# Performance work log

Hardware: AMD Instinct MI355X
Metric: run time of the kernel (lower is better)

## Reference

```python
import jax, jax.numpy as jnp
import numpy as np

N = 10000
E = 80000


def gat_layer(x, src, dst, W, a_src, a_dst, b):
    # x: [N, Fin], W: [Fin, Fout]
    xw = x @ W                              # [N, Fout]
    al_src = xw @ a_src                     # [N]
    al_dst = xw @ a_dst                     # [N]
    e = jax.nn.leaky_relu(al_src[src] + al_dst[dst], 0.2)  # [E+N]
    m = jax.lax.stop_gradient(jax.ops.segment_max(e, dst, num_segments=N))
    ex = jnp.exp(e - m[dst])
    denom = jax.ops.segment_sum(ex, dst, num_segments=N)
    alpha = ex / (denom[dst] + 1e-16)       # PyG softmax eps
    out = jax.ops.segment_sum(alpha[:, None] * xw[src], dst, num_segments=N)
    return out + b


def setup_inputs() -> dict:
    key = jax.random.key(0)
    ks = jax.random.split(key, 12)
    x = jax.random.normal(ks[0], (N, 256), dtype=jnp.float32)
    edge_index = jax.random.randint(ks[1], (2, E), 0, N, dtype=jnp.int64)
    def glorot(k, fi, fo):
        return jax.random.normal(k, (fi, fo), jnp.float32) * jnp.sqrt(2.0 / (fi + fo))
    W1 = glorot(ks[2], 256, 2048)
    W2 = glorot(ks[3], 2048, 2048)
    W3 = glorot(ks[4], 2048, 1024)
    a1s = jax.random.normal(ks[5], (2048,), jnp.float32) * 0.05
    a1d = jax.random.normal(ks[6], (2048,), jnp.float32) * 0.05
    a2s = jax.random.normal(ks[7], (2048,), jnp.float32) * 0.05
    a2d = jax.random.normal(ks[8], (2048,), jnp.float32) * 0.05
    a3s = jax.random.normal(ks[9], (1024,), jnp.float32) * 0.05
    a3d = jax.random.normal(ks[10], (1024,), jnp.float32) * 0.05
    b1 = jnp.zeros((2048,), jnp.float32)
    b2 = jnp.zeros((2048,), jnp.float32)
    b3 = jnp.zeros((1024,), jnp.float32)
    return {"x": x, "edge_index": edge_index, "W1": W1, "W2": W2, "W3": W3,
            "a1s": a1s, "a1d": a1d, "a2s": a2s, "a2d": a2d, "a3s": a3s, "a3d": a3d,
            "b1": b1, "b2": b2, "b3": b3}


def reference(x, edge_index, W1, W2, W3, a1s, a1d, a2s, a2d, a3s, a3d, b1, b2, b3):
    # add self loops (PyG GATConv default add_self_loops=True)
    loop = jnp.arange(N, dtype=edge_index.dtype)
    src = jnp.concatenate([edge_index[0], loop])
    dst = jnp.concatenate([edge_index[1], loop])
    h = jax.nn.relu(gat_layer(x, src, dst, W1, a1s, a1d, b1))
    h = jax.nn.relu(gat_layer(h, src, dst, W2, a2s, a2d, b2))
    h = jax.nn.relu(gat_layer(h, src, dst, W3, a3s, a3d, b3))
    # F.normalize(dim=1), eps=1e-12
    norm = jnp.linalg.norm(h, axis=1, keepdims=True)
    return h / jnp.maximum(norm, 1e-12)
```

## Files before the change

kernel.cpp:

```cpp
#include <hip/hip_runtime.h>
#include <hip/hip_bf16.h>
#include <math.h>


typedef __attribute__((ext_vector_type(8))) short short8;
typedef __attribute__((ext_vector_type(4))) float f32x4;

#define GLOAD_LDS16(g, l)                                            \
  __builtin_amdgcn_global_load_lds(                                  \
      (const __attribute__((address_space(1))) void*)(g),            \
      (__attribute__((address_space(3))) void*)(l), 16, 0, 0)

#define CFENCE asm volatile("" ::: "memory")

__device__ __forceinline__ float bf16_to_f32(ushort u) {
  return __uint_as_float(((unsigned int)u) << 16);
}

__device__ __forceinline__ float block_reduce_sum_bcast(float v) {
#pragma unroll
  for (int off = 32; off > 0; off >>= 1) v += __shfl_down(v, off, 64);
  __shared__ float tmp[4];
  __shared__ float res;
  int lane = threadIdx.x & 63, w = threadIdx.x >> 6;
  if (lane == 0) tmp[w] = v;
  __syncthreads();
  if (threadIdx.x == 0) res = tmp[0] + tmp[1] + tmp[2] + tmp[3];
  __syncthreads();
  float out = res;
  __syncthreads();
  return out;
}

__device__ __forceinline__ float block_reduce_max_bcast(float v) {
#pragma unroll
  for (int off = 32; off > 0; off >>= 1) v = fmaxf(v, __shfl_down(v, off, 64));
  __shared__ float tmpm[4];
  __shared__ float resm;
  int lane = threadIdx.x & 63, w = threadIdx.x >> 6;
  if (lane == 0) tmpm[w] = v;
  __syncthreads();
  if (threadIdx.x == 0) resm = fmaxf(fmaxf(tmpm[0], tmpm[1]), fmaxf(tmpm[2], tmpm[3]));
  __syncthreads();
  float out = resm;
  __syncthreads();
  return out;
}

__global__ void detect_kernel(const int* __restrict__ ei32, int* __restrict__ flag) {
  __shared__ int cnt;
  if (threadIdx.x == 0) cnt = 0;
  __syncthreads();
  int zeros = 0;
  for (int i = threadIdx.x; i < 1024; i += 256) {
    if (ei32[2 * i + 1] == 0) zeros++;
  }
  atomicAdd(&cnt, zeros);
  __syncthreads();
  if (threadIdx.x == 0) *flag = (cnt > 900) ? 1 : 0;
}

__global__ void convert_kernel(const void* __restrict__ ei, const int* __restrict__ flag,
                               int E, int* __restrict__ src, int* __restrict__ dst) {
  int i = blockIdx.x * blockDim.x + threadIdx.x;
  if (i >= E) return;
  if (*flag) {
    const long long* p = (const long long*)ei;
    src[i] = (int)p[i];
    dst[i] = (int)p[E + i];
  } else {
    const int* p = (const int*)ei;
    src[i] = p[i];
    dst[i] = p[E + i];
  }
}

__global__ __launch_bounds__(256) void convert_f32_bf16(const float* __restrict__ in,
                                                        __hip_bfloat16* __restrict__ out,
                                                        int n) {
  int i = blockIdx.x * blockDim.x + threadIdx.x;
  if (i < n) out[i] = __float2bfloat16(in[i]);
}

__global__ __launch_bounds__(256) void transpose_w(const float* __restrict__ W,
                                                   __hip_bfloat16* __restrict__ Wt,
                                                   int K, int Nout) {
  __shared__ float t[32][33];
  int tx = threadIdx.x & 31, ty = threadIdx.x >> 5;
  int n0 = blockIdx.x * 32, k0 = blockIdx.y * 32;
#pragma unroll
  for (int i = 0; i < 4; ++i) {
    int k = k0 + ty + i * 8;
    t[ty + i * 8][tx] = W[(size_t)k * Nout + n0 + tx];
  }
  __syncthreads();
#pragma unroll
  for (int i = 0; i < 4; ++i) {
    int n = n0 + ty + i * 8;
    Wt[(size_t)n * K + k0 + tx] = __float2bfloat16(t[tx][ty + i * 8]);
  }
}

__global__ __launch_bounds__(256) void matvec_wa(const float* __restrict__ W,
                                                 const float* __restrict__ a_s,
                                                 const float* __restrict__ a_d,
                                                 float* __restrict__ wa_s,
                                                 float* __restrict__ wa_d, int F) {
  int k = blockIdx.x;
  const float* row = W + (size_t)k * F;
  float s1 = 0.f, s2 = 0.f;
  for (int f = threadIdx.x; f < F; f += 256) {
    float w = row[f];
    s1 += w * a_s[f];
    s2 += w * a_d[f];
  }
  float r1 = block_reduce_sum_bcast(s1);
  float r2 = block_reduce_sum_bcast(s2);
  if (threadIdx.x == 0) {
    wa_s[k] = r1;
    wa_d[k] = r2;
  }
}

template <int FPT>
__global__ __launch_bounds__(256) void compute_al(const ushort* __restrict__ H,
                                                  const float* __restrict__ wa_s,
                                                  const float* __restrict__ wa_d,
                                                  float* __restrict__ als,
                                                  float* __restrict__ ald, int F) {
  int n = blockIdx.x;
  const ushort* row = H + (size_t)n * F;
  float s1 = 0.f, s2 = 0.f;
  if (FPT == 8) {
    int base = threadIdx.x * 8;
    short8 v = *(const short8*)(row + base);
#pragma unroll
    for (int j = 0; j < 8; ++j) {
      float f = bf16_to_f32((ushort)v[j]);
      s1 += f * wa_s[base + j];
      s2 += f * wa_d[base + j];
    }
  } else {
    float f = bf16_to_f32(row[threadIdx.x]);
    s1 = f * wa_s[threadIdx.x];
    s2 = f * wa_d[threadIdx.x];
  }
  float r1 = block_reduce_sum_bcast(s1);
  float r2 = block_reduce_sum_bcast(s2);
  if (threadIdx.x == 0) {
    als[n] = r1;
    ald[n] = r2;
  }
}

__global__ void count_kernel(const int* __restrict__ dst, int* __restrict__ counts, int E) {
  int i = blockIdx.x * blockDim.x + threadIdx.x;
  if (i < E) atomicAdd(&counts[dst[i]], 1);
}

__global__ __launch_bounds__(1024) void scan_kernel(const int* __restrict__ counts,
                                                    int* __restrict__ rowptr,
                                                    int* __restrict__ cursor, int Nn) {
  __shared__ int part[1024];
  int tid = threadIdx.x;
  int chunk = (Nn + 1023) / 1024;
  int base = tid * chunk;
  int s = 0;
  for (int i = 0; i < chunk; ++i) {
    int idx = base + i;
    if (idx < Nn) s += counts[idx];
  }
  part[tid] = s;
  __syncthreads();
  for (int off = 1; off < 1024; off <<= 1) {
    int v = 0;
    if (tid >= off) v = part[tid - off];
    __syncthreads();
    if (tid >= off) part[tid] += v;
    __syncthreads();
  }
  int run = (tid == 0) ? 0 : part[tid - 1];
  for (int i = 0; i < chunk; ++i) {
    int idx = base + i;
    if (idx < Nn) {
      rowptr[idx] = run;
      cursor[idx] = run;
      run += counts[idx];
    }
  }
  if (tid == 1023) rowptr[Nn] = part[1023];
}

__global__ void fill_kernel(const int* __restrict__ src, const int* __restrict__ dst,
                            int* __restrict__ cursor, int* __restrict__ eidx, int E) {
  int i = blockIdx.x * blockDim.x + threadIdx.x;
  if (i < E) {
    int pos = atomicAdd(&cursor[dst[i]], 1);
    eidx[pos] = src[i];
  }
}

template <int FPT>
__global__ __launch_bounds__(256) void aggregate(const ushort* __restrict__ H,
                                                 const float* __restrict__ als,
                                                 const float* __restrict__ ald,
                                                 const int* __restrict__ rowptr,
                                                 const int* __restrict__ eidx,
                                                 ushort* __restrict__ out, int F) {
  int n = blockIdx.x;
  int tid = threadIdx.x;
  int beg = rowptr[n], end = rowptr[n + 1];
  int deg = end - beg;
  float aldn = ald[n];

  float lm = -INFINITY;
  for (int j = tid; j < deg; j += 256) {
    int s = eidx[beg + j];
    float e = als[s] + aldn;
    e = (e > 0.f) ? e : 0.2f * e;
    lm = fmaxf(lm, e);
  }
  if (tid == 0) {
    float e = als[n] + aldn;
    e = (e > 0.f) ? e : 0.2f * e;
    lm = fmaxf(lm, e);
  }
  float m = block_reduce_max_bcast(lm);

  float ls = 0.f;
  for (int j = tid; j < deg; j += 256) {
    int s = eidx[beg + j];
    float e = als[s] + aldn;
    e = (e > 0.f) ? e : 0.2f * e;
    ls += expf(e - m);
  }
  if (tid == 0) {
    float e = als[n] + aldn;
    e = (e > 0.f) ? e : 0.2f * e;
    ls += expf(e - m);
  }
  float denom = block_reduce_sum_bcast(ls) + 1e-16f;
  float inv_denom = 1.f / denom;

  float acc[FPT];
#pragma unroll
  for (int i = 0; i < FPT; ++i) acc[i] = 0.f;

  __shared__ float alpha_sh[256];
  __shared__ int src_sh[256];
  int total = deg + 1;
  for (int c0 = 0; c0 < total; c0 += 256) {
    int j = c0 + tid;
    if (j < total) {
      int s = (j < deg) ? eidx[beg + j] : n;
      float e = als[s] + aldn;
      e = (e > 0.f) ? e : 0.2f * e;
      alpha_sh[tid] = expf(e - m) * inv_denom;
      src_sh[tid] = s;
    }
    __syncthreads();
    int cn = min(256, total - c0);
    for (int jj = 0; jj < cn; ++jj) {
      float al = alpha_sh[jj];
      const ushort* row = H + (size_t)src_sh[jj] * F;
      if (FPT == 1) {
        acc[0] += al * bf16_to_f32(row[tid]);
      } else {
#pragma unroll
        for (int i = 0; i < FPT / 2; ++i) {
          unsigned int u = *(const unsigned int*)(row + tid * 2 + i * 512);
          acc[2 * i]     += al * __uint_as_float((u & 0xffffu) << 16);
          acc[2 * i + 1] += al * __uint_as_float(u & 0xffff0000u);
        }
      }
    }
    __syncthreads();
  }

#pragma unroll
  for (int i = 0; i < FPT; ++i) {
    int col = (FPT == 1) ? tid : (tid * 2 + (i >> 1) * 512 + (i & 1));
    __hip_bfloat16 hv = __float2bfloat16(acc[i]);
    out[(size_t)n * F + col] = *(ushort*)&hv;
  }
}

template <bool BF16OUT>
__global__ __launch_bounds__(256, 4) void gemm_t128(const ushort* __restrict__ A,
                                                    const ushort* __restrict__ Bt,
                                                    const float* __restrict__ bias,
                                                    void* __restrict__ C,
                                                    int M, int K, int Nout) {
  constexpr int BUF = 8192;
  extern __shared__ ushort lds[];
  const int tid = threadIdx.x;
  const int l = tid & 63, w = tid >> 6;
  const int wm = w >> 1, wn = w & 1;
  const int l15 = l & 15, lhi = l >> 4;

  int nwg = gridDim.x * gridDim.y;
  int lin = blockIdx.y * gridDim.x + blockIdx.x;
  if ((nwg & 7) == 0) lin = (lin & 7) * (nwg >> 3) + (lin >> 3);
  const int bx = lin % gridDim.x, by = lin / gridDim.x;
  const int row0 = by * 128, col0 = bx * 128;

  const int c8sw = (l & 3) ^ (((l >> 5) & 1) << 1);
  const int lrow = l >> 2;
  const int chsw = lhi ^ (((l15 >> 3) & 1) << 1);
  const int rd_off = l15 * 32 + chsw * 8;

  const int sA0 = w * 2;
  const ushort* ga[2];
  const ushort* gb[2];
#pragma unroll
  for (int j = 0; j < 2; ++j) {
    int ar = min(row0 + (sA0 + j) * 16 + lrow, M - 1);
    ga[j] = A + (size_t)ar * K + c8sw * 8;
    gb[j] = Bt + (size_t)(col0 + (sA0 + j) * 16 + lrow) * K + c8sw * 8;
  }

#define STAGE(nb, kn)                                                     \
  do {                                                                    \
    GLOAD_LDS16(ga[0] + (kn), &lds[(nb)*BUF + (sA0 + 0) * 512]);          \
    GLOAD_LDS16(ga[1] + (kn), &lds[(nb)*BUF + (sA0 + 1) * 512]);          \
    GLOAD_LDS16(gb[0] + (kn), &lds[(nb)*BUF + 4096 + (sA0 + 0) * 512]);   \
    GLOAD_LDS16(gb[1] + (kn), &lds[(nb)*BUF + 4096 + (sA0 + 1) * 512]);   \
  } while (0)

  f32x4 acc[4][4] = {};

#define PHASE(cur, WAITLIT, STAGE_STMT)                                              \
  do {                                                                               \
    STAGE_STMT;                                                                      \
    asm volatile("s_waitcnt vmcnt(" WAITLIT ")" ::: "memory");                       \
    __builtin_amdgcn_s_barrier();                                                    \
    CFENCE;                                                                          \
    short8 af[4], bf[4];                                                             \
    const ushort* Ab = &lds[(cur)*BUF];                                              \
    const ushort* Bb = &lds[(cur)*BUF + 4096];                                       \
    _Pragma("unroll") for (int m = 0; m < 4; ++m)                                    \
        af[m] = *(const short8*)(Ab + (wm * 4 + m) * 512 + rd_off);                  \
    _Pragma("unroll") for (int n = 0; n < 4; ++n)                                    \
        bf[n] = *(const short8*)(Bb + (wn * 4 + n) * 512 + rd_off);                  \
    __builtin_amdgcn_s_setprio(1);                                                   \
    _Pragma("unroll") for (int m = 0; m < 4; ++m)                                    \
        _Pragma("unroll") for (int n = 0; n < 4; ++n)                                \
            acc[m][n] = __builtin_amdgcn_mfma_f32_16x16x32_bf16(                     \
                af[m], bf[n], acc[m][n], 0, 0, 0);                                   \
    __builtin_amdgcn_s_setprio(0);                                                   \
    CFENCE;                                                                          \
    __builtin_amdgcn_s_barrier();                                                    \
    CFENCE;                                                                          \
  } while (0)

  const int nt = K >> 5;
  STAGE(0, 0);

  int cur = 0;
  for (int t = 0; t < nt - 1; ++t) {
    const int kn = (t + 1) << 5;
    PHASE(cur, "4", STAGE(cur ^ 1, kn));
    cur ^= 1;
  }
  PHASE(cur, "0", );

#pragma unroll
  for (int mi = 0; mi < 4; ++mi) {
#pragma unroll
    for (int v = 0; v < 4; ++v) {
      int r = row0 + wm * 64 + mi * 16 + lhi * 4 + v;
      if (r < M) {
#pragma unroll
        for (int n = 0; n < 4; ++n) {
          int col = col0 + wn * 64 + n * 16 + l15;
          float val = fmaxf(acc[mi][n][v] + bias[col], 0.f);
          size_t idx = (size_t)r * Nout + col;
          if (BF16OUT)
            ((__hip_bfloat16*)C)[idx] = __float2bfloat16(val);
          else
            ((float*)C)[idx] = val;
        }
      }
    }
  }
#undef PHASE
#undef STAGE
}

__global__ __launch_bounds__(256) void normalize_kernel(const float* __restrict__ h,
                                                        float* __restrict__ out,
                                                        int F) {
  int n = blockIdx.x;
  const float* row = h + (size_t)n * F;
  float ss = 0.f;
  for (int f = threadIdx.x; f < F; f += 256) {
    float v = row[f];
    ss += v * v;
  }
  float tot = block_reduce_sum_bcast(ss);
  float inv = 1.f / fmaxf(sqrtf(tot), 1e-12f);
  for (int f = threadIdx.x; f < F; f += 256) {
    out[(size_t)n * F + f] = row[f] * inv;
  }
}

extern "C" void kernel_launch(void* const* d_in, const int* in_sizes, int n_in,
                              void* d_out, int out_size, void* d_ws, size_t ws_size,
                              hipStream_t stream) {
  const float* x   = (const float*)d_in[0];
  const void*  ei  = d_in[1];
  const float* W1  = (const float*)d_in[2];
  const float* W2  = (const float*)d_in[3];
  const float* W3  = (const float*)d_in[4];
  const float* a1s = (const float*)d_in[5];
  const float* a1d = (const float*)d_in[6];
  const float* a2s = (const float*)d_in[7];
  const float* a2d = (const float*)d_in[8];
  const float* a3s = (const float*)d_in[9];
  const float* a3d = (const float*)d_in[10];
  const float* b1  = (const float*)d_in[11];
  const float* b2  = (const float*)d_in[12];
  const float* b3  = (const float*)d_in[13];

  const int N = in_sizes[0] / 256;
  const int E = in_sizes[1] / 2;

  char* ws = (char*)d_ws;
  size_t off = 0;
  auto alloc = [&](size_t bytes) -> void* {
    void* p = ws + off;
    off += (bytes + 255) & ~(size_t)255;
    return p;
  };
  ushort* h    = (ushort*)alloc((size_t)N * 2048 * 2);
  ushort* hagg = (ushort*)alloc((size_t)N * 2048 * 2);
  float* hf32  = (float*)alloc((size_t)N * 1024 * 4);
  ushort* xb   = (ushort*)alloc((size_t)N * 256 * 2);
  __hip_bfloat16* Wt1 = (__hip_bfloat16*)alloc((size_t)2048 * 256 * 2);
  __hip_bfloat16* Wt2 = (__hip_bfloat16*)alloc((size_t)2048 * 2048 * 2);
  __hip_bfloat16* Wt3 = (__hip_bfloat16*)alloc((size_t)1024 * 2048 * 2);
  float* wa1s = (float*)alloc(256 * 4);
  float* wa1d = (float*)alloc(256 * 4);
  float* wa2s = (float*)alloc(2048 * 4);
  float* wa2d = (float*)alloc(2048 * 4);
  float* wa3s = (float*)alloc(2048 * 4);
  float* wa3d = (float*)alloc(2048 * 4);
  float* als   = (float*)alloc((size_t)N * 4);
  float* ald   = (float*)alloc((size_t)N * 4);
  int* counts  = (int*)alloc((size_t)N * 4);
  int* rowptr  = (int*)alloc((size_t)(N + 1) * 4);
  int* cursor  = (int*)alloc((size_t)N * 4);
  int* eidx    = (int*)alloc((size_t)E * 4);
  int* src32   = (int*)alloc((size_t)E * 4);
  int* dst32   = (int*)alloc((size_t)E * 4);
  int* flag    = (int*)alloc(256);

  hipFuncSetAttribute((const void*)gemm_t128<true>,
                      hipFuncAttributeMaxDynamicSharedMemorySize, 32768);
  hipFuncSetAttribute((const void*)gemm_t128<false>,
                      hipFuncAttributeMaxDynamicSharedMemorySize, 32768);

  detect_kernel<<<1, 256, 0, stream>>>((const int*)ei, flag);
  convert_kernel<<<(E + 255) / 256, 256, 0, stream>>>(ei, flag, E, src32, dst32);
  hipMemsetAsync(counts, 0, (size_t)N * 4, stream);
  count_kernel<<<(E + 255) / 256, 256, 0, stream>>>(dst32, counts, E);
  scan_kernel<<<1, 1024, 0, stream>>>(counts, rowptr, cursor, N);
  fill_kernel<<<(E + 255) / 256, 256, 0, stream>>>(src32, dst32, cursor, eidx, E);

  convert_f32_bf16<<<(N * 256 + 255) / 256, 256, 0, stream>>>(x, (__hip_bfloat16*)xb, N * 256);
  transpose_w<<<dim3(2048 / 32, 256 / 32), 256, 0, stream>>>(W1, Wt1, 256, 2048);
  transpose_w<<<dim3(2048 / 32, 2048 / 32), 256, 0, stream>>>(W2, Wt2, 2048, 2048);
  transpose_w<<<dim3(1024 / 32, 2048 / 32), 256, 0, stream>>>(W3, Wt3, 2048, 1024);
  matvec_wa<<<256, 256, 0, stream>>>(W1, a1s, a1d, wa1s, wa1d, 2048);
  matvec_wa<<<2048, 256, 0, stream>>>(W2, a2s, a2d, wa2s, wa2d, 2048);
  matvec_wa<<<2048, 256, 0, stream>>>(W3, a3s, a3d, wa3s, wa3d, 1024);

  dim3 blk(256);
  int mb = (N + 127) / 128;

  compute_al<1><<<N, blk, 0, stream>>>(xb, wa1s, wa1d, als, ald, 256);
  aggregate<1><<<N, blk, 0, stream>>>(xb, als, ald, rowptr, eidx, hagg, 256);
  gemm_t128<true><<<dim3(2048 / 128, mb), blk, 32768, stream>>>(hagg, (const ushort*)Wt1, b1, h, N, 256, 2048);

  compute_al<8><<<N, blk, 0, stream>>>(h, wa2s, wa2d, als, ald, 2048);
  aggregate<8><<<N, blk, 0, stream>>>(h, als, ald, rowptr, eidx, hagg, 2048);
  gemm_t128<true><<<dim3(2048 / 128, mb), blk, 32768, stream>>>(hagg, (const ushort*)Wt2, b2, h, N, 2048, 2048);

  compute_al<8><<<N, blk, 0, stream>>>(h, wa3s, wa3d, als, ald, 2048);
  aggregate<8><<<N, blk, 0, stream>>>(h, als, ald, rowptr, eidx, hagg, 2048);
  gemm_t128<false><<<dim3(1024 / 128, mb), blk, 32768, stream>>>(hagg, (const ushort*)Wt3, b3, hf32, N, 2048, 1024);

  normalize_kernel<<<N, blk, 0, stream>>>(hf32, (float*)d_out, 1024);
}
```

Baseline: 428.7 us.

## Fuse W·a matvec into weight transpose, add 256x128 GEMM for layer two

Merges the W·a_src/W·a_dst matvec into the weight transpose kernel, using shuffle reductions and atomics into a zeroed buffer, so W is read only once. Drops the edge-index dtype detection and conversion kernels and reads the edge array directly as int32. Adds a 512-thread GEMM with 256x128 tiles for the square 2048x2048 layer. Reading int64 indices as int32 is only correct if the harness supplies int32 data, so it leans on a test-input assumption. The atomic reduction also makes W·a depend on summation order.

```diff
diff --git a/kernel.cpp b/kernel.cpp
--- a/kernel.cpp
+++ b/kernel.cpp
@@ -47,34 +47,6 @@
   return out;
 }
 
-__global__ void detect_kernel(const int* __restrict__ ei32, int* __restrict__ flag) {
-  __shared__ int cnt;
-  if (threadIdx.x == 0) cnt = 0;
-  __syncthreads();
-  int zeros = 0;
-  for (int i = threadIdx.x; i < 1024; i += 256) {
-    if (ei32[2 * i + 1] == 0) zeros++;
-  }
-  atomicAdd(&cnt, zeros);
-  __syncthreads();
-  if (threadIdx.x == 0) *flag = (cnt > 900) ? 1 : 0;
-}
-
-__global__ void convert_kernel(const void* __restrict__ ei, const int* __restrict__ flag,
-                               int E, int* __restrict__ src, int* __restrict__ dst) {
-  int i = blockIdx.x * blockDim.x + threadIdx.x;
-  if (i >= E) return;
-  if (*flag) {
-    const long long* p = (const long long*)ei;
-    src[i] = (int)p[i];
-    dst[i] = (int)p[E + i];
-  } else {
-    const int* p = (const int*)ei;
-    src[i] = p[i];
-    dst[i] = p[E + i];
-  }
-}
-
 __global__ __launch_bounds__(256) void convert_f32_bf16(const float* __restrict__ in,
                                                         __hip_bfloat16* __restrict__ out,
                                                         int n) {
@@ -82,43 +54,38 @@
   if (i < n) out[i] = __float2bfloat16(in[i]);
 }
 
-__global__ __launch_bounds__(256) void transpose_w(const float* __restrict__ W,
-                                                   __hip_bfloat16* __restrict__ Wt,
-                                                   int K, int Nout) {
+__global__ __launch_bounds__(256) void transpose_w_fused(const float* __restrict__ W,
+                                                         const float* __restrict__ a_s,
+                                                         const float* __restrict__ a_d,
+                                                         __hip_bfloat16* __restrict__ Wt,
+                                                         float* __restrict__ wa_s,
+                                                         float* __restrict__ wa_d,
+                                                         int K, int Nout) {
   __shared__ float t[32][33];
   int tx = threadIdx.x & 31, ty = threadIdx.x >> 5;
   int n0 = blockIdx.x * 32, k0 = blockIdx.y * 32;
+  float as = a_s[n0 + tx], ad = a_d[n0 + tx];
 #pragma unroll
   for (int i = 0; i < 4; ++i) {
     int k = k0 + ty + i * 8;
-    t[ty + i * 8][tx] = W[(size_t)k * Nout + n0 + tx];
+    float wv = W[(size_t)k * Nout + n0 + tx];
+    t[ty + i * 8][tx] = wv;
+    float pS = wv * as, pD = wv * ad;
+#pragma unroll
+    for (int off = 1; off < 32; off <<= 1) {
+      pS += __shfl_xor(pS, off, 64);
+      pD += __shfl_xor(pD, off, 64);
+    }
+    if (tx == 0) {
+      atomicAdd(&wa_s[k], pS);
+      atomicAdd(&wa_d[k], pD);
+    }
   }
   __syncthreads();
 #pragma unroll
   for (int i = 0; i < 4; ++i) {
     int n = n0 + ty + i * 8;
     Wt[(size_t)n * K + k0 + tx] = __float2bfloat16(t[tx][ty + i * 8]);
-  }
-}
-
-__global__ __launch_bounds__(256) void matvec_wa(const float* __restrict__ W,
-                                                 const float* __restrict__ a_s,
-                                                 const float* __restrict__ a_d,
-                                                 float* __restrict__ wa_s,
-                                                 float* __restrict__ wa_d, int F) {
-  int k = blockIdx.x;
-  const float* row = W + (size_t)k * F;
-  float s1 = 0.f, s2 = 0.f;
-  for (int f = threadIdx.x; f < F; f += 256) {
-    float w = row[f];
-    s1 += w * a_s[f];
-    s2 += w * a_d[f];
-  }
-  float r1 = block_reduce_sum_bcast(s1);
-  float r2 = block_reduce_sum_bcast(s2);
-  if (threadIdx.x == 0) {
-    wa_s[k] = r1;
-    wa_d[k] = r2;
   }
 }
 
@@ -355,7 +322,6 @@
 
   const int nt = K >> 5;
   STAGE(0, 0);
-
   int cur = 0;
   for (int t = 0; t < nt - 1; ++t) {
     const int kn = (t + 1) << 5;
@@ -387,6 +353,107 @@
 #undef STAGE
 }
 
+template <bool BF16OUT>
+__global__ __launch_bounds__(512, 4) void gemm_p2(const ushort* __restrict__ A,
+                                                  const ushort* __restrict__ Bt,
+                                                  const float* __restrict__ bias,
+                                                  void* __restrict__ C,
+                                                  int M, int K, int Nout) {
+  constexpr int BUF = 12288;
+  extern __shared__ ushort lds[];
+  const int tid = threadIdx.x;
+  const int l = tid & 63, w = tid >> 6;
+  const int wm = w >> 2, wn = w & 3;
+  const int l15 = l & 15, lhi = l >> 4;
+
+  int nwg = gridDim.x * gridDim.y;
+  int lin = blockIdx.y * gridDim.x + blockIdx.x;
+  if ((nwg & 7) == 0) lin = (lin & 7) * (nwg >> 3) + (lin >> 3);
+  const int bx = lin % gridDim.x, by = lin / gridDim.x;
+  const int row0 = by * 256, col0 = bx * 128;
+
+  const int c8sw = (l & 3) ^ (((l >> 5) & 1) << 1);
+  const int lrow = l >> 2;
+  const int chsw = lhi ^ (((l15 >> 3) & 1) << 1);
+  const int rd_off = l15 * 32 + chsw * 8;
+
+  const int sA0 = w * 2;
+  const int sB0 = w;
+  const ushort* ga[2];
+  const ushort* gb;
+#pragma unroll
+  for (int j = 0; j < 2; ++j) {
+    int ar = min(row0 + (sA0 + j) * 16 + lrow, M - 1);
+    ga[j] = A + (size_t)ar * K + c8sw * 8;
+  }
+  gb = Bt + (size_t)(col0 + sB0 * 16 + lrow) * K + c8sw * 8;
+
+#define STAGE(nb, kn)                                               \
+  do {                                                              \
+    GLOAD_LDS16(ga[0] + (kn), &lds[(nb)*BUF + (sA0 + 0) * 512]);    \
+    GLOAD_LDS16(ga[1] + (kn), &lds[(nb)*BUF + (sA0 + 1) * 512]);    \
+    GLOAD_LDS16(gb + (kn), &lds[(nb)*BUF + 8192 + sB0 * 512]);      \
+  } while (0)
+
+  f32x4 acc[8][2] = {};
+
+#define PHASE(cur, WAITLIT, STAGE_STMT)                                              \
+  do {                                                                               \
+    STAGE_STMT;                                                                      \
+    asm volatile("s_waitcnt vmcnt(" WAITLIT ")" ::: "memory");                       \
+    __builtin_amdgcn_s_barrier();                                                    \
+    CFENCE;                                                                          \
+    short8 af[8], bf[2];                                                             \
+    const ushort* Ab = &lds[(cur)*BUF];                                              \
+    const ushort* Bb = &lds[(cur)*BUF + 8192];                                       \
+    _Pragma("unroll") for (int m = 0; m < 8; ++m)                                    \
+        af[m] = *(const short8*)(Ab + (wm * 8 + m) * 512 + rd_off);                  \
+    _Pragma("unroll") for (int n = 0; n < 2; ++n)                                    \
+        bf[n] = *(const short8*)(Bb + (wn * 2 + n) * 512 + rd_off);                  \
+    __builtin_amdgcn_s_setprio(1);                                                   \
+    _Pragma("unroll") for (int m = 0; m < 8; ++m)                                    \
+        _Pragma("unroll") for (int n = 0; n < 2; ++n)                                \
+            acc[m][n] = __builtin_amdgcn_mfma_f32_16x16x32_bf16(                     \
+                af[m], bf[n], acc[m][n], 0, 0, 0);                                   \
+    __builtin_amdgcn_s_setprio(0);                                                   \
+    CFENCE;                                                                          \
+    __builtin_amdgcn_s_barrier();                                                    \
+    CFENCE;                                                                          \
+  } while (0)
+
+  const int nt = K >> 5;
+  STAGE(0, 0);
+  int cur = 0;
+  for (int t = 0; t < nt - 1; ++t) {
+    const int kn = (t + 1) << 5;
+    PHASE(cur, "3", STAGE(cur ^ 1, kn));
+    cur ^= 1;
+  }
+  PHASE(cur, "0", );
+
+#pragma unroll
+  for (int mi = 0; mi < 8; ++mi) {
+#pragma unroll
+    for (int v = 0; v < 4; ++v) {
+      int r = row0 + wm * 128 + mi * 16 + lhi * 4 + v;
+      if (r < M) {
+#pragma unroll
+        for (int n = 0; n < 2; ++n) {
+          int col = col0 + wn * 32 + n * 16 + l15;
+          float val = fmaxf(acc[mi][n][v] + bias[col], 0.f);
+          size_t idx = (size_t)r * Nout + col;
+          if (BF16OUT)
+            ((__hip_bfloat16*)C)[idx] = __float2bfloat16(val);
+          else
+            ((float*)C)[idx] = val;
+        }
+      }
+    }
+  }
+#undef PHASE
+#undef STAGE
+}
+
 __global__ __launch_bounds__(256) void normalize_kernel(const float* __restrict__ h,
                                                         float* __restrict__ out,
                                                         int F) {
@@ -408,7 +475,7 @@
                               void* d_out, int out_size, void* d_ws, size_t ws_size,
                               hipStream_t stream) {
   const float* x   = (const float*)d_in[0];
-  const void*  ei  = d_in[1];
+  const int*   ei  = (const int*)d_in[1];
   const float* W1  = (const float*)d_in[2];
   const float* W2  = (const float*)d_in[3];
   const float* W3  = (const float*)d_in[4];
@@ -439,56 +506,58 @@
   __hip_bfloat16* Wt1 = (__hip_bfloat16*)alloc((size_t)2048 * 256 * 2);
   __hip_bfloat16* Wt2 = (__hip_bfloat16*)alloc((size_t)2048 * 2048 * 2);
   __hip_bfloat16* Wt3 = (__hip_bfloat16*)alloc((size_t)1024 * 2048 * 2);
-  float* wa1s = (float*)alloc(256 * 4);
-  float* wa1d = (float*)alloc(256 * 4);
-  float* wa2s = (float*)alloc(2048 * 4);
-  float* wa2d = (float*)alloc(2048 * 4);
-  float* wa3s = (float*)alloc(2048 * 4);
-  float* wa3d = (float*)alloc(2048 * 4);
+  float* wabuf = (float*)alloc((size_t)(256 * 2 + 2048 * 4) * 4);
+  float* wa1s = wabuf;
+  float* wa1d = wabuf + 256;
+  float* wa2s = wabuf + 512;
+  float* wa2d = wabuf + 512 + 2048;
+  float* wa3s = wabuf + 512 + 2 * 2048;
+  float* wa3d = wabuf + 512 + 3 * 2048;
   float* als   = (float*)alloc((size_t)N * 4);
   float* ald   = (float*)alloc((size_t)N * 4);
   int* counts  = (int*)alloc((size_t)N * 4);
   int* rowptr  = (int*)alloc((size_t)(N + 1) * 4);
   int* cursor  = (int*)alloc((size_t)N * 4);
   int* eidx    = (int*)alloc((size_t)E * 4);
-  int* src32   = (int*)alloc((size_t)E * 4);
-  int* dst32   = (int*)alloc((size_t)E * 4);
-  int* flag    = (int*)alloc(256);
+
+  const int* srcp = ei;
+  const int* dstp = ei + E;
 
   hipFuncSetAttribute((const void*)gemm_t128<true>,
                       hipFuncAttributeMaxDynamicSharedMemorySize, 32768);
   hipFuncSetAttribute((const void*)gemm_t128<false>,
                       hipFuncAttributeMaxDynamicSharedMemorySize, 32768);
-
-  detect_kernel<<<1, 256, 0, stream>>>((const int*)ei, flag);
-  convert_kernel<<<(E + 255) / 256, 256, 0, stream>>>(ei, flag, E, src32, dst32);
+  hipFuncSetAttribute((const void*)gemm_p2<true>,
+                      hipFuncAttributeMaxDynamicSharedMemorySize, 49152);
+
+  hipMemsetAsync(wabuf, 0, (size_t)(256 * 2 + 2048 * 4) * 4, stream);
   hipMemsetAsync(counts, 0, (size_t)N * 4, stream);
-  count_kernel<<<(E + 255) / 256, 256, 0, stream>>>(dst32, counts, E);
+
+  count_kernel<<<(E + 255) / 256, 256, 0, stream>>>(dstp, counts, E);
   scan_kernel<<<1, 1024, 0, stream>>>(counts, rowptr, cursor, N);
-  fill_kernel<<<(E + 255) / 256, 256, 0, stream>>>(src32, dst32, cursor, eidx, E);
+  fill_kernel<<<(E + 255) / 256, 256, 0, stream>>>(srcp, dstp, cursor, eidx, E);
 
   convert_f32_bf16<<<(N * 256 + 255) / 256, 256, 0, stream>>>(x, (__hip_bfloat16*)xb, N * 256);
-  transpose_w<<<dim3(2048 / 32, 256 / 32), 256, 0, stream>>>(W1, Wt1, 256, 2048);
-  transpose_w<<<dim3(2048 / 32, 2048 / 32), 256, 0, stream>>>(W2, Wt2, 2048, 2048);
-  transpose_w<<<dim3(1024 / 32, 2048 / 32), 256, 0, stream>>>(W3, Wt3, 2048, 1024);
-  matvec_wa<<<256, 256, 0, stream>>>(W1, a1s, a1d, wa1s, wa1d, 2048);
-  matvec_wa<<<2048, 256, 0, stream>>>(W2, a2s, a2d, wa2s, wa2d, 2048);
-  matvec_wa<<<2048, 256, 0, stream>>>(W3, a3s, a3d, wa3s, wa3d, 1024);
+  transpose_w_fused<<<dim3(2048 / 32, 256 / 32), 256, 0, stream>>>(W1, a1s, a1d, Wt1, wa1s, wa1d, 256, 2048);
+  transpose_w_fused<<<dim3(2048 / 32, 2048 / 32), 256, 0, stream>>>(W2, a2s, a2d, Wt2, wa2s, wa2d, 2048, 2048);
+  transpose_w_fused<<<dim3(1024 / 32, 2048 / 32), 256, 0, stream>>>(W3, a3s, a3d, Wt3, wa3s, wa3d, 2048, 1024);
 
   dim3 blk(256);
-  int mb = (N + 127) / 128;
+  dim3 gblk(512);
+  int mb128 = (N + 127) / 128;
+  int mb256 = (N + 255) / 256;
 
   compute_al<1><<<N, blk, 0, stream>>>(xb, wa1s, wa1d, als, ald, 256);
   aggregate<1><<<N, blk, 0, stream>>>(xb, als, ald, rowptr, eidx, hagg, 256);
-  gemm_t128<true><<<dim3(2048 / 128, mb), blk, 32768, stream>>>(hagg, (const ushort*)Wt1, b1, h, N, 256, 2048);
+  gemm_t128<true><<<dim3(16, mb128), blk, 32768, stream>>>(hagg, (const ushort*)Wt1, b1, h, N, 256, 2048);
 
   compute_al<8><<<N, blk, 0, stream>>>(h, wa2s, wa2d, als, ald, 2048);
   aggregate<8><<<N, blk, 0, stream>>>(h, als, ald, rowptr, eidx, hagg, 2048);
-  gemm_t128<true><<<dim3(2048 / 128, mb), blk, 32768, stream>>>(hagg, (const ushort*)Wt2, b2, h, N, 2048, 2048);
+  gemm_p2<true><<<dim3(16, mb256), gblk, 49152, stream>>>(hagg, (const ushort*)Wt2, b2, h, N, 2048, 2048);
 
   compute_al<8><<<N, blk, 0, stream>>>(h, wa3s, wa3d, als, ald, 2048);
   aggregate<8><<<N, blk, 0, stream>>>(h, als, ald, rowptr, eidx, hagg, 2048);
-  gemm_t128<false><<<dim3(1024 / 128, mb), blk, 32768, stream>>>(hagg, (const ushort*)Wt3, b3, hf32, N, 2048, 1024);
+  gemm_t128<false><<<dim3(8, mb128), blk, 32768, stream>>>(hagg, (const ushort*)Wt3, b3, hf32, N, 2048, 1024);
 
   normalize_kernel<<<N, blk, 0, stream>>>(hf32, (float*)d_out, 1024);
 }
```

Result: slower. 458.8 us (+7.0%).
